# Kernel tuning notes

Measured on AMD Instinct MI355X. Metric: run time of the kernel, lower is better.

## Reference

```python
import math
import jax, jax.numpy as jnp
import numpy as np

B, T, C = 2, 2048, 2048
NQ, NKV, H = 16, 4, 128
EPS = 1e-6
ROPE_BASE = 5.0e6


def setup_inputs() -> dict:
    key = jax.random.key(0)
    ks = jax.random.split(key, 6)
    x = jax.random.normal(ks[0], (B, T, C), dtype=jnp.float32)
    s = 0.02
    Wq = jax.random.normal(ks[1], (C, NQ * H), dtype=jnp.float32) * s
    Wk = jax.random.normal(ks[2], (C, NKV * H), dtype=jnp.float32) * s
    Wv = jax.random.normal(ks[3], (C, NKV * H), dtype=jnp.float32) * s
    Wo = jax.random.normal(ks[4], (NQ * H, C), dtype=jnp.float32) * s
    q_norm_w = jnp.ones((H,), dtype=jnp.float32)
    k_norm_w = jnp.ones((H,), dtype=jnp.float32)
    # RoPE tables (seq_start = 0)
    inv_freq = 1.0 / (ROPE_BASE ** (jnp.arange(0, H, 2, dtype=jnp.float32) / H))
    t = jnp.arange(T, dtype=jnp.float32)
    freqs = jnp.einsum('i,j->ij', t, inv_freq)          # [T, H/2]
    emb = jnp.concatenate([freqs, freqs], axis=-1)       # [T, H]
    cos = jnp.cos(emb)
    sin = jnp.sin(emb)
    # additive causal mask (finite large negative to stay nan-free)
    causal = jnp.tril(jnp.ones((T, T), dtype=bool))
    attn_mask = jnp.where(causal, 0.0, -1e9).astype(jnp.float32)
    return {"x": x, "Wq": Wq, "Wk": Wk, "Wv": Wv, "Wo": Wo,
            "q_norm_w": q_norm_w, "k_norm_w": k_norm_w,
            "cos": cos, "sin": sin, "attn_mask": attn_mask}


def _rms_norm(x, w):
    # x: [..., H]
    var = jnp.mean(x * x, axis=-1, keepdims=True)
    return w * (x * jax.lax.rsqrt(var + EPS))


def _rotate_half(x):
    x1, x2 = jnp.split(x, 2, axis=-1)
    return jnp.concatenate([-x2, x1], axis=-1)


def reference(x, Wq, Wk, Wv, Wo, q_norm_w, k_norm_w, cos, sin, attn_mask):
    q = (x @ Wq).reshape(B, T, NQ, H)
    k = (x @ Wk).reshape(B, T, NKV, H)
    v = (x @ Wv).reshape(B, T, NKV, H)
    q = _rms_norm(q, q_norm_w)
    k = _rms_norm(k, k_norm_w)
    c = cos[None, :, None, :]  # [1,T,1,H]
    s = sin[None, :, None, :]
    q = q * c + _rotate_half(q) * s
    k = k * c + _rotate_half(k) * s
    rep = NQ // NKV
    k = jnp.repeat(k, rep, axis=2)  # [B,T,NQ,H]
    v = jnp.repeat(v, rep, axis=2)
    scores = jnp.einsum('bihd,bjhd->bhij', q, k) / math.sqrt(H)
    scores = scores + attn_mask[None, None, :, :]
    probs = jax.nn.softmax(scores, axis=-1)
    ctx = jnp.einsum('bhij,bjhd->bihd', probs, v).reshape(B, T, NQ * H)
    return ctx @ Wo
```

## Files before the change

kernel.cpp:

```cpp
#include <hip/hip_runtime.h>
#include <hip/hip_bf16.h>

#define B_   2
#define T_   2048
#define C_   2048
#define NQ_  16
#define NKV_ 4
#define H_   128

using bf16x8 = __attribute__((ext_vector_type(8))) short;
using f32x4  = __attribute__((ext_vector_type(4))) float;

__device__ __forceinline__ unsigned short f2bf(float f) {
    __hip_bfloat16 h = __float2bfloat16(f);
    union { __hip_bfloat16 h; unsigned short s; } c;
    c.h = h;
    return c.s;
}
__device__ __forceinline__ float bf2f(unsigned short s) {
    return __uint_as_float(((unsigned)s) << 16);
}
__device__ __forceinline__ bf16x8 pack8(float4 f0, float4 f1) {
    bf16x8 r;
    r[0] = (short)f2bf(f0.x); r[1] = (short)f2bf(f0.y);
    r[2] = (short)f2bf(f0.z); r[3] = (short)f2bf(f0.w);
    r[4] = (short)f2bf(f1.x); r[5] = (short)f2bf(f1.y);
    r[6] = (short)f2bf(f1.z); r[7] = (short)f2bf(f1.w);
    return r;
}

#define MFMA16(a, b, c) __builtin_amdgcn_mfma_f32_16x16x32_bf16(a, b, c, 0, 0, 0)

__global__ void transpose_cvt(const float* __restrict__ src,
                              unsigned short* __restrict__ dst,
                              int R, int Cc) {
    const int tc = Cc >> 6;
    const int r0 = (blockIdx.x / tc) * 64;
    const int c0 = (blockIdx.x % tc) * 64;
    __shared__ unsigned short Tl[64 * 65];
    const int tid = threadIdx.x;
#pragma unroll
    for (int it = 0; it < 16; ++it) {
        const int idx = it * 256 + tid;
        const int r = idx >> 6, c = idx & 63;
        Tl[c * 65 + r] = f2bf(src[(size_t)(r0 + r) * Cc + c0 + c]);
    }
    __syncthreads();
#pragma unroll
    for (int it = 0; it < 16; ++it) {
        const int idx = it * 256 + tid;
        const int c = idx >> 6, r = idx & 63;
        dst[(size_t)(c0 + c) * R + r0 + r] = Tl[c * 65 + r];
    }
}

#define LDP 40

template <bool A_BF, bool OUT_F32>
__global__ __launch_bounds__(256, 2) void gemm_bt(
    const void* __restrict__ Av,
    const unsigned short* __restrict__ Bt,
    void* __restrict__ Cqv,
    unsigned short* __restrict__ Ck,
    unsigned short* __restrict__ Cv,
    int M, int N, int K, int fused) {
    const int ntn = N >> 7;
    const int tm  = blockIdx.x / ntn;
    const int tn  = blockIdx.x % ntn;

    const int tid  = threadIdx.x;
    const int wv   = tid >> 6;
    const int lane = tid & 63;
    const int col  = lane & 15;
    const int quad = lane >> 4;
    const int wm   = (wv & 1) * 64;
    const int wn   = (wv >> 1) * 64;

    __shared__ unsigned short Al[128 * LDP];
    __shared__ unsigned short Bl[128 * LDP];

    f32x4 acc[4][4];
#pragma unroll
    for (int mt = 0; mt < 4; ++mt)
#pragma unroll
        for (int nt = 0; nt < 4; ++nt) acc[mt][nt] = (f32x4){0.f, 0.f, 0.f, 0.f};

    const int i1 = tid, i2 = tid + 256;
    const size_t aoff1 = (size_t)(tm * 128 + (i1 >> 2)) * K + (i1 & 3) * 8;
    const size_t aoff2 = (size_t)(tm * 128 + (i2 >> 2)) * K + (i2 & 3) * 8;
    const size_t boff1 = (size_t)(tn * 128 + (i1 >> 2)) * K + (i1 & 3) * 8;
    const size_t boff2 = (size_t)(tn * 128 + (i2 >> 2)) * K + (i2 & 3) * 8;
    unsigned short* Aw1 = Al + (i1 >> 2) * LDP + (i1 & 3) * 8;
    unsigned short* Aw2 = Al + (i2 >> 2) * LDP + (i2 & 3) * 8;
    unsigned short* Bw1 = Bl + (i1 >> 2) * LDP + (i1 & 3) * 8;
    unsigned short* Bw2 = Bl + (i2 >> 2) * LDP + (i2 & 3) * 8;

    const unsigned short* Ab16 = (const unsigned short*)Av;
    const float*          Af   = (const float*)Av;

    uint4  a1u, a2u, b1u, b2u;
    float4 a1lo, a1hi, a2lo, a2hi;

    auto loadAB = [&](int kk) {
        if constexpr (A_BF) {
            a1u = *(const uint4*)(Ab16 + aoff1 + kk);
            a2u = *(const uint4*)(Ab16 + aoff2 + kk);
        } else {
            a1lo = *(const float4*)(Af + aoff1 + kk);
            a1hi = *(const float4*)(Af + aoff1 + kk + 4);
            a2lo = *(const float4*)(Af + aoff2 + kk);
            a2hi = *(const float4*)(Af + aoff2 + kk + 4);
        }
        b1u = *(const uint4*)(Bt + boff1 + kk);
        b2u = *(const uint4*)(Bt + boff2 + kk);
    };

    loadAB(0);

    for (int k0 = 0; k0 < K; k0 += 32) {
        __syncthreads();
        if constexpr (A_BF) {
            *(uint4*)Aw1 = a1u;
            *(uint4*)Aw2 = a2u;
        } else {
            *(bf16x8*)Aw1 = pack8(a1lo, a1hi);
            *(bf16x8*)Aw2 = pack8(a2lo, a2hi);
        }
        *(uint4*)Bw1 = b1u;
        *(uint4*)Bw2 = b2u;
        __syncthreads();

        const int kn = (k0 + 32 < K) ? k0 + 32 : k0;
        loadAB(kn);

        bf16x8 af[4], bfv[4];
#pragma unroll
        for (int t = 0; t < 4; ++t) {
            af[t]  = *(const bf16x8*)(Al + (wm + t * 16 + col) * LDP + quad * 8);
            bfv[t] = *(const bf16x8*)(Bl + (wn + t * 16 + col) * LDP + quad * 8);
        }
#pragma unroll
        for (int mt = 0; mt < 4; ++mt)
#pragma unroll
            for (int nt = 0; nt < 4; ++nt)
                acc[mt][nt] = MFMA16(af[mt], bfv[nt], acc[mt][nt]);
    }

    const int nb = tn * 128;
    if constexpr (OUT_F32) {
        float* Co = (float*)Cqv;
#pragma unroll
        for (int mt = 0; mt < 4; ++mt)
#pragma unroll
            for (int nt = 0; nt < 4; ++nt)
#pragma unroll
                for (int r = 0; r < 4; ++r) {
                    const int row = tm * 128 + wm + mt * 16 + quad * 4 + r;
                    const int cc  = nb + wn + nt * 16 + col;
                    Co[(size_t)row * N + cc] = acc[mt][nt][r];
                }
    } else {
        unsigned short* Cb;
        int ldc, nc0;
        if (!fused)         { Cb = (unsigned short*)Cqv; ldc = N;    nc0 = nb;        }
        else if (nb < 2048) { Cb = (unsigned short*)Cqv; ldc = 2048; nc0 = nb;        }
        else if (nb < 2560) { Cb = Ck;                   ldc = 512;  nc0 = nb - 2048; }
        else                { Cb = Cv;                   ldc = 512;  nc0 = nb - 2560; }
#pragma unroll
        for (int mt = 0; mt < 4; ++mt)
#pragma unroll
            for (int nt = 0; nt < 4; ++nt)
#pragma unroll
                for (int r = 0; r < 4; ++r) {
                    const int row = tm * 128 + wm + mt * 16 + quad * 4 + r;
                    const int cc  = nc0 + wn + nt * 16 + col;
                    Cb[(size_t)row * ldc + cc] = f2bf(acc[mt][nt][r]);
                }
    }
}

__global__ void norm_rope(unsigned short* __restrict__ buf,
                          const float* __restrict__ w,
                          const float* __restrict__ cosb,
                          const float* __restrict__ sinb,
                          int nheads, float oscale) {
    const int idx = blockIdx.x;
    const int h   = idx % nheads;
    const int bt  = idx / nheads;
    const int t   = bt % T_;
    unsigned short* row = buf + ((size_t)bt * nheads + h) * H_;
    const int l = threadIdx.x;

    const float x0 = bf2f(row[l]);
    const float x1 = bf2f(row[l + 64]);
    float ss = x0 * x0 + x1 * x1;
#pragma unroll
    for (int off = 32; off; off >>= 1) ss += __shfl_xor(ss, off);
    const float r = rsqrtf(ss * (1.0f / 128.0f) + 1e-6f) * oscale;

    const float n0 = x0 * r * w[l];
    const float n1 = x1 * r * w[l + 64];
    const float c0 = cosb[t * H_ + l];
    const float c1 = cosb[t * H_ + l + 64];
    const float s0 = sinb[t * H_ + l];
    const float s1 = sinb[t * H_ + l + 64];

    row[l]      = f2bf(n0 * c0 - n1 * s0);
    row[l + 64] = f2bf(n1 * c1 + n0 * s1);
}

__global__ __launch_bounds__(512, 2) void flash_attn(
    const unsigned short* __restrict__ qbuf,
    const unsigned short* __restrict__ kbuf,
    const unsigned short* __restrict__ vbuf,
    unsigned short* __restrict__ ctx) {
    const int blk = blockIdx.x;
    const int p   = blk & 7;
    const int h   = (blk >> 3) & 15;
    const int b   = blk >> 7;
    const int kvh = h >> 2;
    const int qtB = 15 - p;

    const int tid  = threadIdx.x;
    const int wave = tid >> 6;
    const int g    = wave >> 2;
    const int gw   = wave & 3;
    const int lane = tid & 63;
    const int col  = lane & 15;
    const int quad = lane >> 4;
    const int gtid = gw * 64 + lane;

    int w0 = (g ? qtB : p) * 128 + gw * 32;
    const int ph1 = 2 * p + 2;

    __shared__ __align__(16) unsigned char smem[109568];
    unsigned short* Kg   = (unsigned short*)smem + g * 8192;
    unsigned short* Vg   = (unsigned short*)(smem + 32768) + g * 9216;
    unsigned short* Pw   = (unsigned short*)(smem + 69632) + wave * 2304;
    float*          alfw = (float*)(smem + 106496) + wave * 32;
    unsigned*       Vw   = (unsigned*)Vg;

    bf16x8 qf[2][4];
    auto loadQ = [&]() {
#pragma unroll
        for (int nt = 0; nt < 2; ++nt)
#pragma unroll
            for (int ks = 0; ks < 4; ++ks) {
                const size_t off =
                    ((size_t)(b * T_ + w0 + nt * 16 + col) * NQ_ + h) * H_ + ks * 32 + quad * 8;
                qf[nt][ks] = *(const bf16x8*)(qbuf + off);
            }
    };
    loadQ();

    f32x4 O[2][8];
#pragma unroll
    for (int pt = 0; pt < 2; ++pt)
#pragma unroll
        for (int dt = 0; dt < 8; ++dt) O[pt][dt] = (f32x4){0.f, 0.f, 0.f, 0.f};
    float m_run[2] = {-3.0e38f, -3.0e38f};
    float l_run[2] = {0.f, 0.f};

    const int swb = (col & 7) << 4;

    uint4 ka[4], va[4];
    const size_t kvstride = (size_t)NKV_ * H_;

    auto issueK = [&](int j0) {
#pragma unroll
        for (int i = 0; i < 4; ++i) {
            const int row = gw * 16 + i * 4 + quad;
            ka[i] = *(const uint4*)(
                kbuf + ((size_t)(b * T_ + j0 + row) * NKV_ + kvh) * H_ +
                ((col ^ (row & 7)) << 3));
        }
    };
    auto issueV = [&](int j0) {
#pragma unroll
        for (int it = 0; it < 2; ++it) {
            const int idx = it * 256 + gtid;
            const int kp  = idx & 31;
            const int dc  = idx >> 5;
            const size_t g0 = ((size_t)(b * T_ + j0 + 2 * kp) * NKV_ + kvh) * H_ + dc * 8;
            va[2 * it]     = *(const uint4*)(vbuf + g0);
            va[2 * it + 1] = *(const uint4*)(vbuf + g0 + kvstride);
        }
    };
    auto writeK = [&]() {
#pragma unroll
        for (int i = 0; i < 4; ++i) {
            const int row = gw * 16 + i * 4 + quad;
            *(uint4*)(Kg + row * 128 + col * 8) = ka[i];
        }
    };
    auto writeV = [&]() {
#pragma unroll
        for (int it = 0; it < 2; ++it) {
            const int idx = it * 256 + gtid;
            const int kp  = idx & 31;
            const int dc  = idx >> 5;
            const uint4 v0 = va[2 * it];
            const uint4 v1 = va[2 * it + 1];
            const int wb = dc * 288 + kp;
            Vw[wb + 0 * 36] = (v0.x & 0xFFFFu) | (v1.x << 16);
            Vw[wb + 1 * 36] = (v0.x >> 16)     | (v1.x & 0xFFFF0000u);
            Vw[wb + 2 * 36] = (v0.y & 0xFFFFu) | (v1.y << 16);
            Vw[wb + 3 * 36] = (v0.y >> 16)     | (v1.y & 0xFFFF0000u);
            Vw[wb + 4 * 36] = (v0.z & 0xFFFFu) | (v1.z << 16);
            Vw[wb + 5 * 36] = (v0.z >> 16)     | (v1.z & 0xFFFF0000u);
            Vw[wb + 6 * 36] = (v0.w & 0xFFFFu) | (v1.w << 16);
            Vw[wb + 7 * 36] = (v0.w >> 16)     | (v1.w & 0xFFFF0000u);
        }
    };

    auto storeOut = [&]() {
        if (quad == 0) {
            alfw[col]      = 1.0f / l_run[0];
            alfw[col + 16] = 1.0f / l_run[1];
        }
        const f32x4 i0 = *(const f32x4*)&alfw[quad * 4];
        const f32x4 i1 = *(const f32x4*)&alfw[quad * 4 + 16];
#pragma unroll
        for (int pt = 0; pt < 2; ++pt)
#pragma unroll
            for (int r = 0; r < 4; ++r) {
                const float inv = pt ? i1[r] : i0[r];
                const int ig = w0 + pt * 16 + quad * 4 + r;
                unsigned short* op = ctx + ((size_t)(b * T_ + ig) * NQ_ + h) * H_;
#pragma unroll
                for (int dt = 0; dt < 8; ++dt)
                    op[dt * 16 + col] = f2bf(O[pt][dt][r] * inv);
            }
    };

    auto chunk_of = [&](int i) { return g ? i : (i < ph1 ? i : i + 15 - 2 * p); };

    issueK(0);
    issueV(0);

    for (int i = 0; i < 17; ++i) {
        const int j0 = chunk_of(i) * 64;
        __syncthreads();
        writeK();
        writeV();
        __syncthreads();

        if (i + 1 < 17) {
            const int jn = chunk_of(i + 1) * 64;
            issueK(jn);
            issueV(jn);
        }

        if (g == 0 && i == ph1) {
            storeOut();
#pragma unroll
            for (int pt = 0; pt < 2; ++pt)
#pragma unroll
                for (int dt = 0; dt < 8; ++dt) O[pt][dt] = (f32x4){0.f, 0.f, 0.f, 0.f};
            m_run[0] = m_run[1] = -3.0e38f;
            l_run[0] = l_run[1] = 0.f;
            w0 = qtB * 128 + gw * 32;
            loadQ();
        }

        if (j0 > w0 + 31) continue;

        f32x4 St[4][2];
#pragma unroll
        for (int mt = 0; mt < 4; ++mt)
#pragma unroll
            for (int nt = 0; nt < 2; ++nt) St[mt][nt] = (f32x4){0.f, 0.f, 0.f, 0.f};
#pragma unroll
        for (int ks = 0; ks < 4; ++ks)
#pragma unroll
            for (int mt = 0; mt < 4; ++mt) {
                const bf16x8 kfrag = *(const bf16x8*)(
                    Kg + ((mt * 16 + col) << 7) + (((ks * 64 + quad * 16) ^ swb) >> 1));
                St[mt][0] = MFMA16(kfrag, qf[0][ks], St[mt][0]);
                St[mt][1] = MFMA16(kfrag, qf[1][ks], St[mt][1]);
            }

        const bool needmask = (j0 + 63 > w0);
        if (needmask) {
            const int ig0 = w0 + col;
#pragma unroll
            for (int mt = 0; mt < 4; ++mt)
#pragma unroll
                for (int r = 0; r < 4; ++r) {
                    const int key = j0 + mt * 16 + quad * 4 + r;
                    if (key > ig0)      St[mt][0][r] = -3.0e38f;
                    if (key > ig0 + 16) St[mt][1][r] = -3.0e38f;
                }
        }

        float rm[2];
#pragma unroll
        for (int nt = 0; nt < 2; ++nt) {
            float m0 = fmaxf(fmaxf(St[0][nt][0], St[0][nt][1]),
                             fmaxf(St[0][nt][2], St[0][nt][3]));
#pragma unroll
            for (int mt = 1; mt < 4; ++mt)
                m0 = fmaxf(m0, fmaxf(fmaxf(St[mt][nt][0], St[mt][nt][1]),
                                     fmaxf(St[mt][nt][2], St[mt][nt][3])));
            m0 = fmaxf(m0, __shfl_xor(m0, 16));
            m0 = fmaxf(m0, __shfl_xor(m0, 32));
            rm[nt] = m0;
        }

        const int defer = __all((rm[0] <= m_run[0] + 8.0f) && (rm[1] <= m_run[1] + 8.0f));
        if (!defer) {
            const float mn0 = fmaxf(m_run[0], rm[0]);
            const float mn1 = fmaxf(m_run[1], rm[1]);
            const float al0 = exp2f(m_run[0] - mn0);
            const float al1 = exp2f(m_run[1] - mn1);
            m_run[0] = mn0; m_run[1] = mn1;
            l_run[0] *= al0; l_run[1] *= al1;
            if (quad == 0) { alfw[col] = al0; alfw[col + 16] = al1; }
        }

        float ls0 = 0.f, ls1 = 0.f;
#pragma unroll
        for (int mt = 0; mt < 4; ++mt) {
            const float p0 = exp2f(St[mt][0][0] - m_run[0]);
            const float p1 = exp2f(St[mt][0][1] - m_run[0]);
            const float p2 = exp2f(St[mt][0][2] - m_run[0]);
            const float p3 = exp2f(St[mt][0][3] - m_run[0]);
            ls0 += (p0 + p1) + (p2 + p3);
            *(uint2*)(Pw + col * 72 + mt * 16 + quad * 4) =
                make_uint2((unsigned)f2bf(p0) | ((unsigned)f2bf(p1) << 16),
                           (unsigned)f2bf(p2) | ((unsigned)f2bf(p3) << 16));
            const float q0 = exp2f(St[mt][1][0] - m_run[1]);
            const float q1 = exp2f(St[mt][1][1] - m_run[1]);
            const float q2 = exp2f(St[mt][1][2] - m_run[1]);
            const float q3 = exp2f(St[mt][1][3] - m_run[1]);
            ls1 += (q0 + q1) + (q2 + q3);
            *(uint2*)(Pw + (col + 16) * 72 + mt * 16 + quad * 4) =
                make_uint2((unsigned)f2bf(q0) | ((unsigned)f2bf(q1) << 16),
                           (unsigned)f2bf(q2) | ((unsigned)f2bf(q3) << 16));
        }
        ls0 += __shfl_xor(ls0, 16); ls0 += __shfl_xor(ls0, 32);
        ls1 += __shfl_xor(ls1, 16); ls1 += __shfl_xor(ls1, 32);
        l_run[0] += ls0; l_run[1] += ls1;

        if (!defer) {
            const f32x4 a0 = *(const f32x4*)&alfw[quad * 4];
            const f32x4 a1 = *(const f32x4*)&alfw[quad * 4 + 16];
#pragma unroll
            for (int dt = 0; dt < 8; ++dt)
#pragma unroll
                for (int r = 0; r < 4; ++r) { O[0][dt][r] *= a0[r]; O[1][dt][r] *= a1[r]; }
        }

#pragma unroll
        for (int ks = 0; ks < 2; ++ks) {
            const bf16x8 pa0 = *(const bf16x8*)(Pw + col * 72 + ks * 32 + quad * 8);
            const bf16x8 pa1 = *(const bf16x8*)(Pw + (col + 16) * 72 + ks * 32 + quad * 8);
#pragma unroll
            for (int dt = 0; dt < 8; ++dt) {
                const bf16x8 vf = *(const bf16x8*)(Vg + (dt * 16 + col) * 72 + ks * 32 + quad * 8);
                O[0][dt] = MFMA16(pa0, vf, O[0][dt]);
                O[1][dt] = MFMA16(pa1, vf, O[1][dt]);
            }
        }
    }

    __syncthreads();
    float* mlA = (float*)(smem + 107520);
    float* mlB = (float*)(smem + 108544);
    if (g == 0) {
        float* Of = (float*)smem + gw * 4096;
        float* ml = mlA + gw * 64;
        if (quad == 0) {
            ml[2 * col]            = m_run[0]; ml[2 * col + 1]        = l_run[0];
            ml[2 * (col + 16)]     = m_run[1]; ml[2 * (col + 16) + 1] = l_run[1];
        }
#pragma unroll
        for (int pt = 0; pt < 2; ++pt)
#pragma unroll
            for (int dt = 0; dt < 8; ++dt)
#pragma unroll
                for (int r = 0; r < 4; ++r)
                    Of[(pt * 16 + quad * 4 + r) * 128 + dt * 16 + col] = O[pt][dt][r];
    }
    __syncthreads();
    if (g == 1) {
        float* Of = (float*)smem + gw * 4096;
        float* mA = mlA + gw * 64;
        float* mB = mlB + gw * 64;
        if (quad == 0) {
            mB[2 * col]            = m_run[0]; mB[2 * col + 1]        = l_run[0];
            mB[2 * (col + 16)]     = m_run[1]; mB[2 * (col + 16) + 1] = l_run[1];
        }
#pragma unroll
        for (int pt = 0; pt < 2; ++pt)
#pragma unroll
            for (int r = 0; r < 4; ++r) {
                const int row = pt * 16 + quad * 4 + r;
                const float mBv = mB[2 * row], lBv = mB[2 * row + 1];
                const float mAv = mA[2 * row], lAv = mA[2 * row + 1];
                const float m  = fmaxf(mAv, mBv);
                const float aB = exp2f(mBv - m);
                const float aA = exp2f(mAv - m);
                const float inv = 1.0f / (lBv * aB + lAv * aA);
                const int ig = w0 + row;
                unsigned short* op = ctx + ((size_t)(b * T_ + ig) * NQ_ + h) * H_;
#pragma unroll
                for (int dt = 0; dt < 8; ++dt)
                    op[dt * 16 + col] =
                        f2bf((O[pt][dt][r] * aB + Of[row * 128 + dt * 16 + col] * aA) * inv);
            }
    }
}

extern "C" void kernel_launch(void* const* d_in, const int* in_sizes, int n_in,
                              void* d_out, int out_size, void* d_ws, size_t ws_size,
                              hipStream_t stream) {
    const float* x    = (const float*)d_in[0];
    const float* Wq   = (const float*)d_in[1];
    const float* Wk   = (const float*)d_in[2];
    const float* Wv   = (const float*)d_in[3];
    const float* Wo   = (const float*)d_in[4];
    const float* qnw  = (const float*)d_in[5];
    const float* knw  = (const float*)d_in[6];
    const float* cosb = (const float*)d_in[7];
    const float* sinb = (const float*)d_in[8];

    const int M = B_ * T_;
    unsigned short* ws  = (unsigned short*)d_ws;
    unsigned short* WqT = ws;
    unsigned short* WkT = WqT + (size_t)2048 * 2048;
    unsigned short* WvT = WkT + (size_t)512 * 2048;
    unsigned short* ctx = ws;
    unsigned short* q   = ws + (size_t)8388608;
    unsigned short* k   = ws + (size_t)16777216;
    unsigned short* v   = ws + (size_t)18874368;
    unsigned short* WoT = q;

    transpose_cvt<<<(2048 / 64) * (2048 / 64), 256, 0, stream>>>(Wq, WqT, 2048, 2048);
    transpose_cvt<<<(2048 / 64) * (512 / 64),  256, 0, stream>>>(Wk, WkT, 2048, 512);
    transpose_cvt<<<(2048 / 64) * (512 / 64),  256, 0, stream>>>(Wv, WvT, 2048, 512);

    gemm_bt<false, false><<<(M / 128) * (3072 / 128), 256, 0, stream>>>(
        (const void*)x, WqT, (void*)q, k, v, M, 3072, C_, 1);

    norm_rope<<<M * NQ_, 64, 0, stream>>>(q, qnw, cosb, sinb, NQ_, 0.12751743f);
    norm_rope<<<M * NKV_, 64, 0, stream>>>(k, knw, cosb, sinb, NKV_, 1.0f);

    flash_attn<<<256, 512, 0, stream>>>(q, k, v, ctx);

    transpose_cvt<<<(2048 / 64) * (2048 / 64), 256, 0, stream>>>(Wo, WoT, 2048, 2048);
    gemm_bt<true, true><<<(M / 128) * (C_ / 128), 256, 0, stream>>>(
        (const void*)ctx, WoT, d_out, nullptr, nullptr, M, C_, NQ_ * H_, 0);
}
```

Measured before the change: 396.2 us.

## Load K fragments directly from global into registers, drop K LDS staging

K tiles are now read straight from global memory into MFMA-ready register fragments (each wave loads the full 64x128 K chunk itself) instead of being staged cooperatively through shared memory. The next chunk's K is prefetched right after the QK^T MFMAs. This removes the K LDS writes and reads and shrinks shared memory from about 107KB to 75KB, which could allow higher occupancy. In exchange, each of the 8 waves redundantly loads the whole K tile from global/L2, and register pressure goes up by 16 bf16x8 fragments.

Result: no change. 396.4 us (+0.1%).

```diff
diff --git a/kernel.cpp b/kernel.cpp
--- a/kernel.cpp
+++ b/kernel.cpp
@@ -233,11 +233,10 @@
     int w0 = (g ? qtB : p) * 128 + gw * 32;
     const int ph1 = 2 * p + 2;
 
-    __shared__ __align__(16) unsigned char smem[109568];
-    unsigned short* Kg   = (unsigned short*)smem + g * 8192;
-    unsigned short* Vg   = (unsigned short*)(smem + 32768) + g * 9216;
-    unsigned short* Pw   = (unsigned short*)(smem + 69632) + wave * 2304;
-    float*          alfw = (float*)(smem + 106496) + wave * 32;
+    __shared__ __align__(16) unsigned char smem[76800];
+    unsigned short* Vg   = (unsigned short*)smem + g * 9216;
+    unsigned short* Pw   = (unsigned short*)(smem + 36864) + wave * 2304;
+    float*          alfw = (float*)(smem + 73728) + wave * 32;
     unsigned*       Vw   = (unsigned*)Vg;
 
     bf16x8 qf[2][4];
@@ -261,20 +260,21 @@
     float m_run[2] = {-3.0e38f, -3.0e38f};
     float l_run[2] = {0.f, 0.f};
 
-    const int swb = (col & 7) << 4;
-
-    uint4 ka[4], va[4];
+    bf16x8 kf[4][4];
+    const unsigned short* kb = kbuf + ((size_t)(b * T_) * NKV_ + kvh) * H_;
+    const int koff = col * (NKV_ * H_) + quad * 8;
+    auto loadK = [&](int j0) {
+#pragma unroll
+        for (int mt = 0; mt < 4; ++mt) {
+            const unsigned short* kr = kb + (size_t)((j0 + mt * 16) * (NKV_ * H_) + koff);
+#pragma unroll
+            for (int ks = 0; ks < 4; ++ks)
+                kf[mt][ks] = *(const bf16x8*)(kr + ks * 32);
+        }
+    };
+
+    uint4 va[4];
     const size_t kvstride = (size_t)NKV_ * H_;
-
-    auto issueK = [&](int j0) {
-#pragma unroll
-        for (int i = 0; i < 4; ++i) {
-            const int row = gw * 16 + i * 4 + quad;
-            ka[i] = *(const uint4*)(
-                kbuf + ((size_t)(b * T_ + j0 + row) * NKV_ + kvh) * H_ +
-                ((col ^ (row & 7)) << 3));
-        }
-    };
     auto issueV = [&](int j0) {
 #pragma unroll
         for (int it = 0; it < 2; ++it) {
@@ -284,13 +284,6 @@
             const size_t g0 = ((size_t)(b * T_ + j0 + 2 * kp) * NKV_ + kvh) * H_ + dc * 8;
             va[2 * it]     = *(const uint4*)(vbuf + g0);
             va[2 * it + 1] = *(const uint4*)(vbuf + g0 + kvstride);
-        }
-    };
-    auto writeK = [&]() {
-#pragma unroll
-        for (int i = 0; i < 4; ++i) {
-            const int row = gw * 16 + i * 4 + quad;
-            *(uint4*)(Kg + row * 128 + col * 8) = ka[i];
         }
     };
     auto writeV = [&]() {
@@ -335,21 +328,16 @@
 
     auto chunk_of = [&](int i) { return g ? i : (i < ph1 ? i : i + 15 - 2 * p); };
 
-    issueK(0);
+    loadK(0);
     issueV(0);
 
     for (int i = 0; i < 17; ++i) {
         const int j0 = chunk_of(i) * 64;
         __syncthreads();
-        writeK();
         writeV();
         __syncthreads();
 
-        if (i + 1 < 17) {
-            const int jn = chunk_of(i + 1) * 64;
-            issueK(jn);
-            issueV(jn);
-        }
+        if (i + 1 < 17) issueV(chunk_of(i + 1) * 64);
 
         if (g == 0 && i == ph1) {
             storeOut();
@@ -363,22 +351,26 @@
             loadQ();
         }
 
-        if (j0 > w0 + 31) continue;
+        const bool act = (j0 <= w0 + 31);
 
         f32x4 St[4][2];
-#pragma unroll
-        for (int mt = 0; mt < 4; ++mt)
-#pragma unroll
-            for (int nt = 0; nt < 2; ++nt) St[mt][nt] = (f32x4){0.f, 0.f, 0.f, 0.f};
-#pragma unroll
-        for (int ks = 0; ks < 4; ++ks)
-#pragma unroll
-            for (int mt = 0; mt < 4; ++mt) {
-                const bf16x8 kfrag = *(const bf16x8*)(
-                    Kg + ((mt * 16 + col) << 7) + (((ks * 64 + quad * 16) ^ swb) >> 1));
-                St[mt][0] = MFMA16(kfrag, qf[0][ks], St[mt][0]);
-                St[mt][1] = MFMA16(kfrag, qf[1][ks], St[mt][1]);
-            }
+        if (act) {
+#pragma unroll
+            for (int mt = 0; mt < 4; ++mt)
+#pragma unroll
+                for (int nt = 0; nt < 2; ++nt) St[mt][nt] = (f32x4){0.f, 0.f, 0.f, 0.f};
+#pragma unroll
+            for (int ks = 0; ks < 4; ++ks)
+#pragma unroll
+                for (int mt = 0; mt < 4; ++mt) {
+                    St[mt][0] = MFMA16(kf[mt][ks], qf[0][ks], St[mt][0]);
+                    St[mt][1] = MFMA16(kf[mt][ks], qf[1][ks], St[mt][1]);
+                }
+        }
+
+        if (i + 1 < 17) loadK(chunk_of(i + 1) * 64);
+
+        if (!act) continue;
 
         const bool needmask = (j0 + 63 > w0);
         if (needmask) {
@@ -465,8 +457,8 @@
     }
 
     __syncthreads();
-    float* mlA = (float*)(smem + 107520);
-    float* mlB = (float*)(smem + 108544);
+    float* mlA = (float*)(smem + 74752);
+    float* mlB = (float*)(smem + 75776);
     if (g == 0) {
         float* Of = (float*)smem + gw * 4096;
         float* ml = mlA + gw * 64;
```
